# Performance work log

Measured on AMD Instinct MI355X. Metric: run time of the kernel, lower is better.

Reference implementation:

```python
import jax, jax.numpy as jnp
import numpy as np

B, S, L, D, M = 32, 256, 64, 100, 20  # batch, n_sentences, max_sentence_len, embed_dim, n_memories


def setup_inputs() -> dict:
    key = jax.random.key(0)
    ks = jax.random.split(key, 6)
    batch = jax.random.normal(ks[0], (B, S, L, D), dtype=jnp.float32)
    enc_mult = jnp.ones((L, D), dtype=jnp.float32)  # input_encoder_multiplier (init to ones)
    keys = 0.1 * jax.random.normal(ks[1], (M, D), dtype=jnp.float32)
    U = 0.1 * jax.random.normal(ks[2], (D, D), dtype=jnp.float32)  # nn.Linear weight [out,in]
    V = 0.1 * jax.random.normal(ks[3], (D, D), dtype=jnp.float32)
    W = 0.1 * jax.random.normal(ks[4], (D, D), dtype=jnp.float32)
    prelu_a = jnp.ones((), dtype=jnp.float32)  # PReLU(init=1), single shared parameter
    return {"batch": batch, "enc_mult": enc_mult, "keys": keys, "U": U, "V": V, "W": W, "prelu_a": prelu_a}


def reference(batch, enc_mult, keys, U, V, W, prelu_a):
    # Encode: elementwise multiply by learned positional multiplier, sum over words -> [B, S, D]
    enc = (batch * enc_mult).sum(axis=2)

    def prelu(x):
        return jnp.where(x >= 0, x, prelu_a * x)

    # keys @ V.T is step-invariant
    keysV = jnp.einsum('md,ed->me', keys, V)  # [M, D]

    def step(mem, s):  # mem: [B, M, D], s: [B, D]
        memory_gate = jnp.einsum('bd,bmd->bm', s, mem)          # [B, M]
        key_gate = jnp.einsum('bd,md->bm', s, keys)              # [B, M]
        gate = jax.nn.sigmoid(memory_gate + key_gate)            # [B, M]
        cand = prelu(
            jnp.einsum('bmd,ed->bme', mem, U)                    # U(memories)
            + keysV[None, :, :]                                  # V(keys)
            + jnp.einsum('bd,ed->be', s, W)[:, None, :]          # W(sentence), broadcast over M
        )
        mem = mem + cand * gate[:, :, None]
        mem = mem / jnp.linalg.norm(mem, axis=2, keepdims=True)  # L2 normalize each memory slot
        return mem, None

    mem0 = jnp.broadcast_to(keys[None, :, :], (B, M, D))  # memories init = keys repeated per batch
    mem_final, _ = jax.lax.scan(step, mem0, jnp.swapaxes(enc, 0, 1))  # scan over sentences
    return mem_final
```

## Files before the change

kernel.cpp:

```cpp
#include <hip/hip_runtime.h>


typedef float v2f __attribute__((ext_vector_type(2)));

__global__ __launch_bounds__(64) void encode_k(
    const float* __restrict__ batch,
    const float* __restrict__ encm,
    float* __restrict__ enc)
{
    __shared__ float4 stage[1600];
    __shared__ float4 part[50];
    const int lane = threadIdx.x;
    float4 MU[25];
    const float4* e4 = (const float4*)encm;
    #pragma unroll
    for (int i = 0; i < 25; ++i) MU[i] = e4[i * 64 + lane];
    const int q = (lane >= 25) ? 1 : 0;
    const int c = lane - 25 * q;
    const bool red = (lane < 50);

    for (int r8 = 0; r8 < 8; ++r8) {
        const int row = blockIdx.x * 8 + r8;
        const float4* rb = (const float4*)batch + (size_t)row * 1600;
        #pragma unroll
        for (int i = 0; i < 25; ++i) {
            float4 x = rb[i * 64 + lane];
            float4 mu = MU[i];
            float4 p;
            p.x = x.x * mu.x; p.y = x.y * mu.y; p.z = x.z * mu.z; p.w = x.w * mu.w;
            stage[i * 64 + lane] = p;
        }
        __syncthreads();
        float4 a0 = {0.f,0.f,0.f,0.f}, a1 = {0.f,0.f,0.f,0.f};
        if (red) {
            const int l0 = 32 * q;
            #pragma unroll
            for (int k = 0; k < 32; k += 2) {
                float4 u = stage[(l0 + k) * 25 + c];
                float4 v = stage[(l0 + k + 1) * 25 + c];
                a0.x += u.x; a0.y += u.y; a0.z += u.z; a0.w += u.w;
                a1.x += v.x; a1.y += v.y; a1.z += v.z; a1.w += v.w;
            }
            float4 s;
            s.x = a0.x + a1.x; s.y = a0.y + a1.y; s.z = a0.z + a1.z; s.w = a0.w + a1.w;
            part[lane] = s;
        }
        __syncthreads();
        if (lane < 25) {
            float4 s = part[lane], t2 = part[lane + 25];
            float4 o;
            o.x = s.x + t2.x; o.y = s.y + t2.y; o.z = s.z + t2.z; o.w = s.w + t2.w;
            ((float4*)enc)[(size_t)row * 25 + lane] = o;
        }
        __syncthreads();
    }
}

__global__ __launch_bounds__(128) void project_k(
    const float* __restrict__ enc,
    const float* __restrict__ W,
    const float* __restrict__ keys,
    float* __restrict__ sWp,
    float* __restrict__ kg)
{
    const int t = threadIdx.x;
    if (t >= 120) return;
    const float* wrow = (t < 100) ? (W + t * 100) : (keys + (t - 100) * 100);
    const int row0 = blockIdx.x * 4;
    const float4* w4 = (const float4*)wrow;
    const float4* e0 = (const float4*)(enc + (size_t)row0 * 100);
    const float4* e1 = e0 + 25;
    const float4* e2 = e0 + 50;
    const float4* e3 = e0 + 75;
    float a0 = 0.f, a1 = 0.f, a2 = 0.f, a3 = 0.f;
    #pragma unroll
    for (int k = 0; k < 25; ++k) {
        float4 w = w4[k];
        float4 s0 = e0[k], s1 = e1[k], s2 = e2[k], s3 = e3[k];
        a0 += w.x * s0.x + w.y * s0.y + w.z * s0.z + w.w * s0.w;
        a1 += w.x * s1.x + w.y * s1.y + w.z * s1.z + w.w * s1.w;
        a2 += w.x * s2.x + w.y * s2.y + w.z * s2.z + w.w * s2.w;
        a3 += w.x * s3.x + w.y * s3.y + w.z * s3.z + w.w * s3.w;
    }
    if (t < 100) {
        sWp[(size_t)row0 * 100 + t]       = a0;
        sWp[(size_t)(row0 + 1) * 100 + t] = a1;
        sWp[(size_t)(row0 + 2) * 100 + t] = a2;
        sWp[(size_t)(row0 + 3) * 100 + t] = a3;
    } else {
        const int m = t - 100;
        kg[(size_t)row0 * 20 + m]       = a0;
        kg[(size_t)(row0 + 1) * 20 + m] = a1;
        kg[(size_t)(row0 + 2) * 20 + m] = a2;
        kg[(size_t)(row0 + 3) * 20 + m] = a3;
    }
}

template <int CTRL>
__device__ __forceinline__ float dpp_add_f(float x) {
    int s = __builtin_amdgcn_update_dpp(0, __float_as_int(x), CTRL, 0xF, 0xF, true);
    return x + __int_as_float(s);
}
__device__ __forceinline__ float lane63(float x) {
    return __int_as_float(__builtin_amdgcn_readlane(__float_as_int(x), 63));
}

__global__ __launch_bounds__(64, 1) void entnet_scan(
    const float* __restrict__ enc,
    const float* __restrict__ sWp,
    const float* __restrict__ kg,
    const float* __restrict__ keys,
    const float* __restrict__ U,
    const float* __restrict__ V,
    const float* __restrict__ paPtr,
    float* __restrict__ out)
{
    __shared__ float4 mem4[32];
    float* memF = (float*)mem4;
    const int lane = threadIdx.x;
    const int b = blockIdx.x / 20;
    const int m = blockIdx.x % 20;
    const bool hi = (lane < 36);
    const float h = hi ? 1.f : 0.f;
    const int e0 = lane;
    const int e1 = hi ? (64 + lane) : 99;
    const float pa = paPtr[0];

    v2f Upk[100];
    {
        const float4* u0 = (const float4*)(U + e0 * 100);
        const float4* u1 = (const float4*)(U + e1 * 100);
        #pragma unroll
        for (int k = 0; k < 25; ++k) {
            float4 a = u0[k], c = u1[k];
            Upk[4 * k + 0] = (v2f){a.x, c.x};
            Upk[4 * k + 1] = (v2f){a.y, c.y};
            Upk[4 * k + 2] = (v2f){a.z, c.z};
            Upk[4 * k + 3] = (v2f){a.w, c.w};
        }
    }
    float kv0 = 0.f, kv1 = 0.f;
    {
        const float4* km = (const float4*)(keys + m * 100);
        const float4* v0 = (const float4*)(V + e0 * 100);
        const float4* v1 = (const float4*)(V + e1 * 100);
        #pragma unroll
        for (int k = 0; k < 25; ++k) {
            float4 kk = km[k], a = v0[k], c = v1[k];
            kv0 += a.x * kk.x + a.y * kk.y + a.z * kk.z + a.w * kk.w;
            kv1 += c.x * kk.x + c.y * kk.y + c.z * kk.z + c.w * kk.w;
        }
    }
    const float k0 = keys[m * 100 + e0];
    const float k1 = h * keys[m * 100 + e1];
    float nm0 = k0, nm1 = k1;
    memF[lane] = nm0;
    memF[64 + lane] = nm1;
    __asm__ __volatile__("" ::: "memory");

    float nq = k0 * k0 + k1 * k1;
    nq = dpp_add_f<0x111>(nq); nq = dpp_add_f<0x112>(nq); nq = dpp_add_f<0x114>(nq);
    nq = dpp_add_f<0x118>(nq); nq = dpp_add_f<0x142>(nq); nq = dpp_add_f<0x143>(nq);
    float nsq = lane63(nq);
    float rn = 1.f;

    const float* encRow = enc + (size_t)b * 25600;
    const float* sWRow  = sWp + (size_t)b * 25600;
    const float* kgRow  = kg + (size_t)b * 5120 + m;

    float sv0 = encRow[e0], sv1 = encRow[e1];
    float sw0 = sWRow[e0],  sw1 = sWRow[e1];
    float kgc = kgRow[0];

    for (int step = 0; step < 256; ++step) {
        const int nxt = (step < 255 ? step + 1 : 255);
        const float nsv0 = encRow[nxt * 100 + e0], nsv1 = encRow[nxt * 100 + e1];
        const float nsw0 = sWRow[nxt * 100 + e0], nsw1 = sWRow[nxt * 100 + e1];
        const float nkg  = kgRow[nxt * 20];

        v2f A0 = {0.f,0.f}, A1 = {0.f,0.f}, A2 = {0.f,0.f}, A3 = {0.f,0.f}, A4 = {0.f,0.f};
        #pragma unroll
        for (int k = 0; k < 25; k += 5) {
            float4 v0 = mem4[k],     v1 = mem4[k + 1], v2 = mem4[k + 2];
            float4 v3 = mem4[k + 3], v4 = mem4[k + 4];
            A0 += Upk[4*k+0]*v0.x;      A0 += Upk[4*k+1]*v0.y;      A0 += Upk[4*k+2]*v0.z;      A0 += Upk[4*k+3]*v0.w;
            A1 += Upk[4*(k+1)+0]*v1.x;  A1 += Upk[4*(k+1)+1]*v1.y;  A1 += Upk[4*(k+1)+2]*v1.z;  A1 += Upk[4*(k+1)+3]*v1.w;
            A2 += Upk[4*(k+2)+0]*v2.x;  A2 += Upk[4*(k+2)+1]*v2.y;  A2 += Upk[4*(k+2)+2]*v2.z;  A2 += Upk[4*(k+2)+3]*v2.w;
            A3 += Upk[4*(k+3)+0]*v3.x;  A3 += Upk[4*(k+3)+1]*v3.y;  A3 += Upk[4*(k+3)+2]*v3.z;  A3 += Upk[4*(k+3)+3]*v3.w;
            A4 += Upk[4*(k+4)+0]*v4.x;  A4 += Upk[4*(k+4)+1]*v4.y;  A4 += Upk[4*(k+4)+2]*v4.z;  A4 += Upk[4*(k+4)+3]*v4.w;
        }
        v2f acc = ((A0 + A1) + (A2 + A3)) + A4;

        float x0 = rn * acc.x + kv0 + sw0;
        float x1 = rn * acc.y + kv1 + sw1;
        float c0 = (x0 >= 0.f) ? x0 : pa * x0;
        float c1 = (x1 >= 0.f) ? x1 : pa * x1;
        c1 *= h;

        float q1 = sv0 * nm0 + sv1 * nm1;
        float q3 = nm0 * c0 + nm1 * c1;
        float p4 = c0 * c0 + c1 * c1;
        #define RND3(C) q1 = dpp_add_f<C>(q1); q3 = dpp_add_f<C>(q3); p4 = dpp_add_f<C>(p4);
        RND3(0x111) RND3(0x112) RND3(0x114) RND3(0x118) RND3(0x142) RND3(0x143)
        #undef RND3
        const float Q1 = lane63(q1);
        const float Q3 = lane63(q3);
        const float P4 = lane63(p4);

        const float g = 1.f / (1.f + __expf(-(rn * Q1 + kgc)));

        nm0 = rn * nm0 + g * c0;
        nm1 = rn * nm1 + g * c1;
        memF[lane] = nm0;
        memF[64 + lane] = nm1;
        __asm__ __volatile__("" ::: "memory");

        const float grn = g * rn;
        const float n2 = nsq + 2.f * grn * Q3 + g * g * P4;
        rn = rsqrtf(n2);
        nsq = 1.f;

        sv0 = nsv0; sv1 = nsv1; sw0 = nsw0; sw1 = nsw1; kgc = nkg;
    }
    float* orow = out + (size_t)(b * 20 + m) * 100;
    orow[e0] = nm0 * rn;
    if (hi) orow[e1] = nm1 * rn;
}

extern "C" void kernel_launch(void* const* d_in, const int* in_sizes, int n_in,
                              void* d_out, int out_size, void* d_ws, size_t ws_size,
                              hipStream_t stream) {
    const float* batch = (const float*)d_in[0];
    const float* encm  = (const float*)d_in[1];
    const float* keys  = (const float*)d_in[2];
    const float* U     = (const float*)d_in[3];
    const float* V     = (const float*)d_in[4];
    const float* W     = (const float*)d_in[5];
    const float* pa    = (const float*)d_in[6];
    float* out = (float*)d_out;

    float* enc = (float*)d_ws;
    float* sWp = enc + 819200;
    float* kgb = sWp + 819200;

    encode_k<<<1024, 64, 0, stream>>>(batch, encm, enc);
    project_k<<<2048, 128, 0, stream>>>(enc, W, keys, sWp, kgb);
    entnet_scan<<<640, 64, 0, stream>>>(enc, sWp, kgb, keys, U, V, pa, out);
}
```

Baseline: 554.9 us.

## Track U·mem linearly via candidate matvec, simplify encode, transpose projection weights

The scan now keeps P = U·(unnormalized memory) and updates it as P = rn*P + g*U·cand. The U matvec on the candidate can then be issued right after the candidate is formed and overlap the gate reductions, which removes the matvec-then-gate serial dependency on each step. The encode kernel becomes a simple per-thread strided reduction with no LDS staging. The projection kernel reads a transposed W/keys table built by a new prep kernel and stages enc rows in shared memory, so its weight loads are coalesced. The linear recurrence on P may accumulate rounding drift over 256 steps.

Result: faster. 529.5 us (-4.6%).

```diff
diff --git a/kernel.cpp b/kernel.cpp
--- a/kernel.cpp
+++ b/kernel.cpp
@@ -3,91 +3,67 @@
 
 typedef float v2f __attribute__((ext_vector_type(2)));
 
-__global__ __launch_bounds__(64) void encode_k(
+__global__ __launch_bounds__(256) void encode_k(
     const float* __restrict__ batch,
     const float* __restrict__ encm,
     float* __restrict__ enc)
 {
-    __shared__ float4 stage[1600];
-    __shared__ float4 part[50];
-    const int lane = threadIdx.x;
-    float4 MU[25];
-    const float4* e4 = (const float4*)encm;
-    #pragma unroll
-    for (int i = 0; i < 25; ++i) MU[i] = e4[i * 64 + lane];
-    const int q = (lane >= 25) ? 1 : 0;
-    const int c = lane - 25 * q;
-    const bool red = (lane < 50);
-
-    for (int r8 = 0; r8 < 8; ++r8) {
-        const int row = blockIdx.x * 8 + r8;
-        const float4* rb = (const float4*)batch + (size_t)row * 1600;
-        #pragma unroll
-        for (int i = 0; i < 25; ++i) {
-            float4 x = rb[i * 64 + lane];
-            float4 mu = MU[i];
-            float4 p;
-            p.x = x.x * mu.x; p.y = x.y * mu.y; p.z = x.z * mu.z; p.w = x.w * mu.w;
-            stage[i * 64 + lane] = p;
-        }
-        __syncthreads();
-        float4 a0 = {0.f,0.f,0.f,0.f}, a1 = {0.f,0.f,0.f,0.f};
-        if (red) {
-            const int l0 = 32 * q;
-            #pragma unroll
-            for (int k = 0; k < 32; k += 2) {
-                float4 u = stage[(l0 + k) * 25 + c];
-                float4 v = stage[(l0 + k + 1) * 25 + c];
-                a0.x += u.x; a0.y += u.y; a0.z += u.z; a0.w += u.w;
-                a1.x += v.x; a1.y += v.y; a1.z += v.z; a1.w += v.w;
-            }
-            float4 s;
-            s.x = a0.x + a1.x; s.y = a0.y + a1.y; s.z = a0.z + a1.z; s.w = a0.w + a1.w;
-            part[lane] = s;
-        }
-        __syncthreads();
-        if (lane < 25) {
-            float4 s = part[lane], t2 = part[lane + 25];
-            float4 o;
-            o.x = s.x + t2.x; o.y = s.y + t2.y; o.z = s.z + t2.z; o.w = s.w + t2.w;
-            ((float4*)enc)[(size_t)row * 25 + lane] = o;
-        }
-        __syncthreads();
-    }
+    const int tid = blockIdx.x * 256 + threadIdx.x;
+    const int r = tid / 25;
+    const int c = tid % 25;
+    const float4* b4 = (const float4*)batch + (size_t)r * 1600 + c;
+    const float4* e4 = (const float4*)encm + c;
+    float4 a0 = {0.f,0.f,0.f,0.f}, a1 = {0.f,0.f,0.f,0.f};
+    #pragma unroll 8
+    for (int l = 0; l < 64; l += 2) {
+        float4 x0 = b4[l * 25],       mu0 = e4[l * 25];
+        float4 x1 = b4[(l + 1) * 25], mu1 = e4[(l + 1) * 25];
+        a0.x += x0.x * mu0.x; a0.y += x0.y * mu0.y; a0.z += x0.z * mu0.z; a0.w += x0.w * mu0.w;
+        a1.x += x1.x * mu1.x; a1.y += x1.y * mu1.y; a1.z += x1.z * mu1.z; a1.w += x1.w * mu1.w;
+    }
+    float4 s;
+    s.x = a0.x + a1.x; s.y = a0.y + a1.y; s.z = a0.z + a1.z; s.w = a0.w + a1.w;
+    ((float4*)enc)[(size_t)r * 25 + c] = s;
+}
+
+__global__ void prep_k(const float* __restrict__ W,
+                       const float* __restrict__ keys,
+                       float* __restrict__ T)
+{
+    const int d = blockIdx.x;
+    const int e = threadIdx.x;
+    float v = 0.f;
+    if (e < 100) v = W[e * 100 + d];
+    else if (e < 120) v = keys[(e - 100) * 100 + d];
+    T[d * 128 + e] = v;
 }
 
 __global__ __launch_bounds__(128) void project_k(
     const float* __restrict__ enc,
-    const float* __restrict__ W,
-    const float* __restrict__ keys,
+    const float* __restrict__ T,
     float* __restrict__ sWp,
     float* __restrict__ kg)
 {
+    __shared__ float encS[400];
     const int t = threadIdx.x;
-    if (t >= 120) return;
-    const float* wrow = (t < 100) ? (W + t * 100) : (keys + (t - 100) * 100);
     const int row0 = blockIdx.x * 4;
-    const float4* w4 = (const float4*)wrow;
-    const float4* e0 = (const float4*)(enc + (size_t)row0 * 100);
-    const float4* e1 = e0 + 25;
-    const float4* e2 = e0 + 50;
-    const float4* e3 = e0 + 75;
+    if (t < 100) ((float4*)encS)[t] = ((const float4*)(enc + (size_t)row0 * 100))[t];
+    __syncthreads();
     float a0 = 0.f, a1 = 0.f, a2 = 0.f, a3 = 0.f;
-    #pragma unroll
-    for (int k = 0; k < 25; ++k) {
-        float4 w = w4[k];
-        float4 s0 = e0[k], s1 = e1[k], s2 = e2[k], s3 = e3[k];
-        a0 += w.x * s0.x + w.y * s0.y + w.z * s0.z + w.w * s0.w;
-        a1 += w.x * s1.x + w.y * s1.y + w.z * s1.z + w.w * s1.w;
-        a2 += w.x * s2.x + w.y * s2.y + w.z * s2.z + w.w * s2.w;
-        a3 += w.x * s3.x + w.y * s3.y + w.z * s3.z + w.w * s3.w;
+    #pragma unroll 4
+    for (int d = 0; d < 100; ++d) {
+        const float w = T[d * 128 + t];
+        a0 += w * encS[d];
+        a1 += w * encS[100 + d];
+        a2 += w * encS[200 + d];
+        a3 += w * encS[300 + d];
     }
     if (t < 100) {
         sWp[(size_t)row0 * 100 + t]       = a0;
         sWp[(size_t)(row0 + 1) * 100 + t] = a1;
         sWp[(size_t)(row0 + 2) * 100 + t] = a2;
         sWp[(size_t)(row0 + 3) * 100 + t] = a3;
-    } else {
+    } else if (t < 120) {
         const int m = t - 100;
         kg[(size_t)row0 * 20 + m]       = a0;
         kg[(size_t)(row0 + 1) * 20 + m] = a1;
@@ -104,6 +80,20 @@
 __device__ __forceinline__ float lane63(float x) {
     return __int_as_float(__builtin_amdgcn_readlane(__float_as_int(x), 63));
 }
+
+#define MATVEC100(RES, SRC4)                                                   \
+    {                                                                          \
+        v2f A0 = {0.f,0.f}, A1 = {0.f,0.f}, A2 = {0.f,0.f}, A3 = {0.f,0.f};    \
+        _Pragma("unroll")                                                      \
+        for (int k = 0; k < 25; ++k) {                                         \
+            float4 v = (SRC4)[k];                                              \
+            A0 += Upk[4 * k + 0] * v.x;                                        \
+            A1 += Upk[4 * k + 1] * v.y;                                        \
+            A2 += Upk[4 * k + 2] * v.z;                                        \
+            A3 += Upk[4 * k + 3] * v.w;                                        \
+        }                                                                      \
+        RES = (A0 + A1) + (A2 + A3);                                           \
+    }
 
 __global__ __launch_bounds__(64, 1) void entnet_scan(
     const float* __restrict__ enc,
@@ -115,8 +105,8 @@
     const float* __restrict__ paPtr,
     float* __restrict__ out)
 {
-    __shared__ float4 mem4[32];
-    float* memF = (float*)mem4;
+    __shared__ float4 cand4[32];
+    float* candF = (float*)cand4;
     const int lane = threadIdx.x;
     const int b = blockIdx.x / 20;
     const int m = blockIdx.x % 20;
@@ -154,9 +144,12 @@
     const float k0 = keys[m * 100 + e0];
     const float k1 = h * keys[m * 100 + e1];
     float nm0 = k0, nm1 = k1;
-    memF[lane] = nm0;
-    memF[64 + lane] = nm1;
+    candF[lane] = nm0;
+    candF[64 + lane] = nm1;
     __asm__ __volatile__("" ::: "memory");
+
+    v2f P;
+    MATVEC100(P, cand4);
 
     float nq = k0 * k0 + k1 * k1;
     nq = dpp_add_f<0x111>(nq); nq = dpp_add_f<0x112>(nq); nq = dpp_add_f<0x114>(nq);
@@ -178,24 +171,15 @@
         const float nsw0 = sWRow[nxt * 100 + e0], nsw1 = sWRow[nxt * 100 + e1];
         const float nkg  = kgRow[nxt * 20];
 
-        v2f A0 = {0.f,0.f}, A1 = {0.f,0.f}, A2 = {0.f,0.f}, A3 = {0.f,0.f}, A4 = {0.f,0.f};
-        #pragma unroll
-        for (int k = 0; k < 25; k += 5) {
-            float4 v0 = mem4[k],     v1 = mem4[k + 1], v2 = mem4[k + 2];
-            float4 v3 = mem4[k + 3], v4 = mem4[k + 4];
-            A0 += Upk[4*k+0]*v0.x;      A0 += Upk[4*k+1]*v0.y;      A0 += Upk[4*k+2]*v0.z;      A0 += Upk[4*k+3]*v0.w;
-            A1 += Upk[4*(k+1)+0]*v1.x;  A1 += Upk[4*(k+1)+1]*v1.y;  A1 += Upk[4*(k+1)+2]*v1.z;  A1 += Upk[4*(k+1)+3]*v1.w;
-            A2 += Upk[4*(k+2)+0]*v2.x;  A2 += Upk[4*(k+2)+1]*v2.y;  A2 += Upk[4*(k+2)+2]*v2.z;  A2 += Upk[4*(k+2)+3]*v2.w;
-            A3 += Upk[4*(k+3)+0]*v3.x;  A3 += Upk[4*(k+3)+1]*v3.y;  A3 += Upk[4*(k+3)+2]*v3.z;  A3 += Upk[4*(k+3)+3]*v3.w;
-            A4 += Upk[4*(k+4)+0]*v4.x;  A4 += Upk[4*(k+4)+1]*v4.y;  A4 += Upk[4*(k+4)+2]*v4.z;  A4 += Upk[4*(k+4)+3]*v4.w;
-        }
-        v2f acc = ((A0 + A1) + (A2 + A3)) + A4;
-
-        float x0 = rn * acc.x + kv0 + sw0;
-        float x1 = rn * acc.y + kv1 + sw1;
+        const float x0 = rn * P.x + kv0 + sw0;
+        const float x1 = rn * P.y + kv1 + sw1;
         float c0 = (x0 >= 0.f) ? x0 : pa * x0;
         float c1 = (x1 >= 0.f) ? x1 : pa * x1;
         c1 *= h;
+
+        candF[lane] = c0;
+        candF[64 + lane] = c1;
+        __asm__ __volatile__("" ::: "memory");
 
         float q1 = sv0 * nm0 + sv1 * nm1;
         float q3 = nm0 * c0 + nm1 * c1;
@@ -203,6 +187,10 @@
         #define RND3(C) q1 = dpp_add_f<C>(q1); q3 = dpp_add_f<C>(q3); p4 = dpp_add_f<C>(p4);
         RND3(0x111) RND3(0x112) RND3(0x114) RND3(0x118) RND3(0x142) RND3(0x143)
         #undef RND3
+
+        v2f Q;
+        MATVEC100(Q, cand4);
+
         const float Q1 = lane63(q1);
         const float Q3 = lane63(q3);
         const float P4 = lane63(p4);
@@ -211,12 +199,9 @@
 
         nm0 = rn * nm0 + g * c0;
         nm1 = rn * nm1 + g * c1;
-        memF[lane] = nm0;
-        memF[64 + lane] = nm1;
-        __asm__ __volatile__("" ::: "memory");
-
-        const float grn = g * rn;
-        const float n2 = nsq + 2.f * grn * Q3 + g * g * P4;
+        P = rn * P + g * Q;
+
+        const float n2 = nsq + 2.f * (g * rn) * Q3 + g * g * P4;
         rn = rsqrtf(n2);
         nsq = 1.f;
 
@@ -242,8 +227,10 @@
     float* enc = (float*)d_ws;
     float* sWp = enc + 819200;
     float* kgb = sWp + 819200;
-
-    encode_k<<<1024, 64, 0, stream>>>(batch, encm, enc);
-    project_k<<<2048, 128, 0, stream>>>(enc, W, keys, sWp, kgb);
+    float* T   = kgb + 163840;
+
+    encode_k<<<800, 256, 0, stream>>>(batch, encm, enc);
+    prep_k<<<100, 128, 0, stream>>>(W, keys, T);
+    project_k<<<2048, 128, 0, stream>>>(enc, T, sWp, kgb);
     entnet_scan<<<640, 64, 0, stream>>>(enc, sWp, kgb, keys, U, V, pa, out);
 }
```
